# Kernel tuning notes

Hardware: AMD Instinct MI355X
Metric: run time of the kernel (lower is better)

The kernel has to match this reference:

```python
import jax, jax.numpy as jnp
import numpy as np

B = 2048            # number of session graphs in the batch
ORDER = 3           # multi-order granularities s1, s2, s3
D = 128             # input_dim = hidden_dim = output_dim (fc_out is None)
NODES_PER = (50, 25, 16)   # nodes per graph for s1, s2, s3
NPG = sum(NODES_PER)       # 91 nodes per graph (summed batch_num_nodes)
N = B * NPG                # total flattened nodes


def setup_inputs() -> dict:
    key = jax.random.key(0)
    k0, k1, k2, k3 = jax.random.split(key, 4)
    feats = jax.random.normal(k0, (N, D), dtype=jnp.float32)
    scale = 1.0 / np.sqrt(D).astype(np.float32)
    Wu = jax.random.normal(k1, (ORDER, D, D), dtype=jnp.float32) * scale
    bu = jnp.zeros((ORDER, D), dtype=jnp.float32)
    Wv = jax.random.normal(k2, (ORDER, D, D), dtype=jnp.float32) * scale
    We = jax.random.normal(k3, (ORDER, D), dtype=jnp.float32) * scale
    # segment id per node: idx = cat([ones(batch_num_nodes[j]) * j])
    idx = jnp.repeat(jnp.arange(B, dtype=jnp.int32), NPG)
    # last node of each order's block inside every graph (feats['s_i'][last_nodess[i]])
    offs = np.cumsum([0] + list(NODES_PER))
    last = np.stack([np.arange(B) * NPG + (offs[o + 1] - 1) for o in range(ORDER)])
    last_idx = jnp.asarray(last, dtype=jnp.int32)  # [ORDER, B]
    return {"feats": feats, "Wu": Wu, "bu": bu, "Wv": Wv, "We": We,
            "idx": idx, "last_idx": last_idx}


def reference(feats, Wu, bu, Wv, We, idx, last_idx):
    # feat_u = fc_u[i](feats)                        -> [O, N, D]
    feat_u = jnp.einsum('nd,odh->onh', feats, Wu) + bu[:, None, :]
    # feat_v = fc_v[i](feat_vs[:, i])[idx]           -> [O, N, D]
    fv = jnp.einsum('obd,odh->obh', feats[last_idx], Wv)   # [O, B, D]
    feat_v = fv[:, idx, :]                                  # gather per segment id
    # e = fc_e[i](sigmoid(feat_u + feat_v))          -> [N, O]
    e = jnp.einsum('onh,oh->no', jax.nn.sigmoid(feat_u + feat_v), We)
    # alpha = segment_softmax(batch_num_nodes, e), numerically stable
    m = jax.lax.stop_gradient(jax.ops.segment_max(e, idx, num_segments=B))
    ex = jnp.exp(e - m[idx])
    denom = jax.ops.segment_sum(ex, idx, num_segments=B)
    alpha = ex / denom[idx]                                 # [N, O]
    # rst = segment_reduce(batch_num_nodes, feats * alpha, 'sum') -> [B, O, D]
    weighted = alpha[:, :, None] * feats[:, None, :]        # [N, O, D]
    rst = jax.ops.segment_sum(weighted, idx, num_segments=B)
    return rst  # [B, ORDER, D]; fc_out is None and activation is None
```

## Files before the change

### kernel.cpp

```cpp
#include <hip/hip_runtime.h>
#include <hip/hip_bf16.h>
#include <stdint.h>

#define NB 2048
#define D 128
#define NPG 91

typedef __attribute__((ext_vector_type(8))) short short8;
typedef __attribute__((ext_vector_type(4))) float f32x4;

__device__ __forceinline__ unsigned bf16pk(float a, float b) {
  __hip_bfloat162 h2 = __float22bfloat162_rn(make_float2(a, b));
  return *reinterpret_cast<unsigned*>(&h2);
}

__device__ __forceinline__ float sigf(float x) {
  float e = __expf(-x);
  return __builtin_amdgcn_rcpf(1.0f + e);
}

__global__ void w_pack(const float* __restrict__ Wu,
                       const float* __restrict__ Wv,
                       uint4* __restrict__ wpk) {
  const int u = blockIdx.x;
  const float* W = (u < 12) ? Wu : Wv;
  const int uu = (u < 12) ? u : u - 12;
  const int o = uu >> 2, kk = uu & 3;
  const int t = threadIdx.x;
  #pragma unroll
  for (int i = 0; i < 2; ++i) {
    int idx = i * 256 + t;
    int row = idx >> 2, g = idx & 3;
    const float* src = W + (size_t)o * D * D + (kk * 32 + g * 8) * D + row;
    uint4 pk;
    pk.x = bf16pk(src[0 * D], src[1 * D]);
    pk.y = bf16pk(src[2 * D], src[3 * D]);
    pk.z = bf16pk(src[4 * D], src[5 * D]);
    pk.w = bf16pk(src[6 * D], src[7 * D]);
    wpk[(size_t)u * 512 + idx] = pk;
  }
}

__global__ __launch_bounds__(512, 8) void sihg_main(
    const float* __restrict__ feats,
    const uint4* __restrict__ wpk,
    const float* __restrict__ bu,
    const float* __restrict__ We,
    float* __restrict__ out) {
  __shared__ __align__(16) char lds[38528];
  constexpr int FE_OFF  = 0;
  constexpr int BFV_OFF = 24576;
  constexpr int BUL_OFF = 25088;
  constexpr int WEL_OFF = 26624;
  constexpr int EP_OFF  = 28160;
  constexpr int AL_OFF  = 37376;

  const int t = threadIdx.x;
  const int b = blockIdx.x;
  const int q = t >> 6;
  const int l = t & 63;
  const int g = l >> 4;
  const int lm = l & 15;

  float* bfvp = (float*)(lds + BFV_OFF);
  float* bul = (float*)(lds + BUL_OFF);
  float* wel = (float*)(lds + WEL_OFF);
  float (*ep)[3][96] = (float (*)[3][96])(lds + EP_OFF);
  float (*alpha)[96] = (float (*)[96])(lds + AL_OFF);

  const float* fbase = feats + (size_t)b * NPG * D;

  #pragma unroll 1
  for (int i = 0; i < 3; ++i) {
    int c = t + i * 512;
    int r = c >> 4, d0 = (c & 15) * 8;
    uint4 pk4;
    if (r < NPG) {
      const float* src = fbase + r * D + d0;
      float4 f0 = *(const float4*)(src);
      float4 f1 = *(const float4*)(src + 4);
      pk4.x = bf16pk(f0.x, f0.y);
      pk4.y = bf16pk(f0.z, f0.w);
      pk4.z = bf16pk(f1.x, f1.y);
      pk4.w = bf16pk(f1.z, f1.w);
    } else {
      pk4.x = 0u; pk4.y = 0u; pk4.z = 0u; pk4.w = 0u;
    }
    int off = r * 256 + ((d0 * 2) ^ ((r & 7) << 4));
    *(uint4*)(lds + FE_OFF + off) = pk4;
  }
  if (t < 384) {
    bul[t] = bu[t];
    wel[t] = We[t];
  }
  __syncthreads();

  const int LROW[3] = {49, 74, 90};

  #pragma unroll 1
  for (int o = 0; o < 3; ++o) {
    {
      const int frow = LROW[o];
      const int fswz = (frow & 7) << 4;
      f32x4 z = {0.f, 0.f, 0.f, 0.f};
      #pragma unroll
      for (int kk = 0; kk < 4; ++kk) {
        short8 av = *(const short8*)&wpk[(size_t)(12 + o * 4 + kk) * 512 + (q * 16 + lm) * 4 + g];
        short8 bv = *(const short8*)(lds + FE_OFF + frow * 256 + ((kk * 64 + g * 16) ^ fswz));
        z = __builtin_amdgcn_mfma_f32_16x16x32_bf16(av, bv, z, 0, 0, 0);
      }
      if (lm == 0) {
        #pragma unroll
        for (int r = 0; r < 4; ++r)
          bfvp[q * 16 + g * 4 + r] = z[r] + bul[o * 128 + q * 16 + g * 4 + r];
      }
    }
    __syncthreads();

    short8 a[4];
    #pragma unroll
    for (int kk = 0; kk < 4; ++kk)
      a[kk] = *(const short8*)&wpk[(size_t)(o * 4 + kk) * 512 + (q * 16 + lm) * 4 + g];

    #pragma unroll 1
    for (int nh = 0; nh < 2; ++nh) {
      f32x4 acc[3];
      #pragma unroll
      for (int j = 0; j < 3; ++j) acc[j] = (f32x4){0.f, 0.f, 0.f, 0.f};

      #pragma unroll
      for (int kk = 0; kk < 4; ++kk) {
        const int cb = kk * 64 + g * 16;
        #pragma unroll
        for (int j = 0; j < 3; ++j) {
          const int nt = nh * 3 + j;
          short8 bfr = *(const short8*)(lds + FE_OFF + (nt * 16 + lm) * 256 + (cb ^ ((lm & 7) << 4)));
          acc[j] = __builtin_amdgcn_mfma_f32_16x16x32_bf16(a[kk], bfr, acc[j], 0, 0, 0);
        }
      }
      const float* bbp = &bfvp[q * 16 + g * 4];
      const float* wwp = &wel[o * 128 + q * 16 + g * 4];
      #pragma unroll
      for (int j = 0; j < 3; ++j) {
        float e = 0.f;
        #pragma unroll
        for (int r = 0; r < 4; ++r)
          e += sigf(acc[j][r] + bbp[r]) * wwp[r];
        e += __shfl_xor(e, 16);
        e += __shfl_xor(e, 32);
        if (l < 16) ep[q][o][(nh * 3 + j) * 16 + l] = e;
      }
    }
    if (o < 2) __syncthreads();
  }
  __syncthreads();

  if (q < 3) {
    const int o = q;
    const int n1 = l, n2 = l + 64;
    float e1 = -1e30f, e2 = -1e30f;
    if (n1 < NPG) {
      e1 = 0.f;
      #pragma unroll
      for (int j = 0; j < 8; ++j) e1 += ep[j][o][n1];
    }
    if (n2 < NPG) {
      e2 = 0.f;
      #pragma unroll
      for (int j = 0; j < 8; ++j) e2 += ep[j][o][n2];
    }
    float mx = fmaxf(e1, e2);
    #pragma unroll
    for (int m = 1; m < 64; m <<= 1) mx = fmaxf(mx, __shfl_xor(mx, m));
    float x1 = (n1 < NPG) ? __expf(e1 - mx) : 0.f;
    float x2 = (n2 < NPG) ? __expf(e2 - mx) : 0.f;
    float s = x1 + x2;
    #pragma unroll
    for (int m = 1; m < 64; m <<= 1) s += __shfl_xor(s, m);
    float inv = __builtin_amdgcn_rcpf(s);
    if (n1 < NPG) alpha[o][n1] = x1 * inv;
    if (n2 < NPG) alpha[o][n2] = x2 * inv;
  }
  __syncthreads();

  {
    const int hw = t >> 5;
    const int d4 = (t & 31) * 4;
    float a0x = 0.f, a0y = 0.f, a0z = 0.f, a0w = 0.f;
    float a1x = 0.f, a1y = 0.f, a1z = 0.f, a1w = 0.f;
    float a2x = 0.f, a2y = 0.f, a2z = 0.f, a2w = 0.f;
    #pragma unroll 1
    for (int n = hw; n < NPG; n += 16) {
      float4 f = *(const float4*)(fbase + n * D + d4);
      float al0 = alpha[0][n], al1 = alpha[1][n], al2 = alpha[2][n];
      a0x += f.x * al0; a0y += f.y * al0; a0z += f.z * al0; a0w += f.w * al0;
      a1x += f.x * al1; a1y += f.y * al1; a1z += f.z * al1; a1w += f.w * al1;
      a2x += f.x * al2; a2y += f.y * al2; a2z += f.z * al2; a2w += f.w * al2;
    }
    a0x += __shfl_xor(a0x, 32); a0y += __shfl_xor(a0y, 32);
    a0z += __shfl_xor(a0z, 32); a0w += __shfl_xor(a0w, 32);
    a1x += __shfl_xor(a1x, 32); a1y += __shfl_xor(a1y, 32);
    a1z += __shfl_xor(a1z, 32); a1w += __shfl_xor(a1w, 32);
    a2x += __shfl_xor(a2x, 32); a2y += __shfl_xor(a2y, 32);
    a2z += __shfl_xor(a2z, 32); a2w += __shfl_xor(a2w, 32);
    float* part = (float*)(lds + FE_OFF);
    if (l < 32) {
      float4 s0 = {a0x, a0y, a0z, a0w};
      float4 s1 = {a1x, a1y, a1z, a1w};
      float4 s2 = {a2x, a2y, a2z, a2w};
      *(float4*)&part[q * 384 + 0 * 128 + d4] = s0;
      *(float4*)&part[q * 384 + 1 * 128 + d4] = s1;
      *(float4*)&part[q * 384 + 2 * 128 + d4] = s2;
    }
  }
  __syncthreads();
  if (t < 384) {
    const float* part = (const float*)(lds + FE_OFF);
    float s = 0.f;
    #pragma unroll
    for (int j = 0; j < 8; ++j) s += part[j * 384 + t];
    out[(size_t)b * 384 + t] = s;
  }
}

extern "C" void kernel_launch(void* const* d_in, const int* in_sizes, int n_in,
                              void* d_out, int out_size, void* d_ws, size_t ws_size,
                              hipStream_t stream) {
  const float* feats = (const float*)d_in[0];
  const float* Wu    = (const float*)d_in[1];
  const float* bu    = (const float*)d_in[2];
  const float* Wv    = (const float*)d_in[3];
  const float* We    = (const float*)d_in[4];
  float* out = (float*)d_out;
  uint4* wpk = (uint4*)d_ws;

  w_pack<<<24, 256, 0, stream>>>(Wu, Wv, wpk);
  sihg_main<<<NB, 512, 0, stream>>>(feats, wpk, bu, We, out);
}
```

Measured before the change: 65.23 us.

## Hoist feat_v projections for all orders before main loop, drop per-order barriers

Computes the fv projection for all three orders up front into a 384-entry LDS buffer, so a single barrier replaces the two per-order barriers in the main loop. The inner loop now processes all six node tiles at once with six accumulators, loading each weight fragment inline rather than keeping four preloaded. Bias is read directly from global memory with vector loads instead of being staged in LDS. This reduces synchronisation and loop overhead, at the cost of more live accumulator registers, which could lower occupancy.

Measured after the change: 174.5 us. 2.67x slower.

```diff
diff --git a/kernel.cpp b/kernel.cpp
--- a/kernel.cpp
+++ b/kernel.cpp
@@ -47,13 +47,12 @@
     const float* __restrict__ bu,
     const float* __restrict__ We,
     float* __restrict__ out) {
-  __shared__ __align__(16) char lds[38528];
+  __shared__ __align__(16) char lds[38016];
   constexpr int FE_OFF  = 0;
   constexpr int BFV_OFF = 24576;
-  constexpr int BUL_OFF = 25088;
-  constexpr int WEL_OFF = 26624;
-  constexpr int EP_OFF  = 28160;
-  constexpr int AL_OFF  = 37376;
+  constexpr int WEL_OFF = 26112;
+  constexpr int EP_OFF  = 27648;
+  constexpr int AL_OFF  = 36864;
 
   const int t = threadIdx.x;
   const int b = blockIdx.x;
@@ -63,7 +62,6 @@
   const int lm = l & 15;
 
   float* bfvp = (float*)(lds + BFV_OFF);
-  float* bul = (float*)(lds + BUL_OFF);
   float* wel = (float*)(lds + WEL_OFF);
   float (*ep)[3][96] = (float (*)[3][96])(lds + EP_OFF);
   float (*alpha)[96] = (float (*)[96])(lds + AL_OFF);
@@ -89,17 +87,13 @@
     int off = r * 256 + ((d0 * 2) ^ ((r & 7) << 4));
     *(uint4*)(lds + FE_OFF + off) = pk4;
   }
-  if (t < 384) {
-    bul[t] = bu[t];
-    wel[t] = We[t];
-  }
-  __syncthreads();
-
-  const int LROW[3] = {49, 74, 90};
-
-  #pragma unroll 1
-  for (int o = 0; o < 3; ++o) {
-    {
+  if (t < 384) wel[t] = We[t];
+  __syncthreads();
+
+  {
+    const int LROW[3] = {49, 74, 90};
+    #pragma unroll
+    for (int o = 0; o < 3; ++o) {
       const int frow = LROW[o];
       const int fswz = (frow & 7) << 4;
       f32x4 z = {0.f, 0.f, 0.f, 0.f};
@@ -110,48 +104,43 @@
         z = __builtin_amdgcn_mfma_f32_16x16x32_bf16(av, bv, z, 0, 0, 0);
       }
       if (lm == 0) {
-        #pragma unroll
-        for (int r = 0; r < 4; ++r)
-          bfvp[q * 16 + g * 4 + r] = z[r] + bul[o * 128 + q * 16 + g * 4 + r];
+        f32x4 bb = *(const f32x4*)&bu[o * 128 + q * 16 + g * 4];
+        f32x4 s = {z[0] + bb[0], z[1] + bb[1], z[2] + bb[2], z[3] + bb[3]};
+        *(f32x4*)&bfvp[o * 128 + q * 16 + g * 4] = s;
       }
     }
-    __syncthreads();
-
-    short8 a[4];
-    #pragma unroll
-    for (int kk = 0; kk < 4; ++kk)
-      a[kk] = *(const short8*)&wpk[(size_t)(o * 4 + kk) * 512 + (q * 16 + lm) * 4 + g];
-
-    #pragma unroll 1
-    for (int nh = 0; nh < 2; ++nh) {
-      f32x4 acc[3];
-      #pragma unroll
-      for (int j = 0; j < 3; ++j) acc[j] = (f32x4){0.f, 0.f, 0.f, 0.f};
-
-      #pragma unroll
-      for (int kk = 0; kk < 4; ++kk) {
-        const int cb = kk * 64 + g * 16;
-        #pragma unroll
-        for (int j = 0; j < 3; ++j) {
-          const int nt = nh * 3 + j;
-          short8 bfr = *(const short8*)(lds + FE_OFF + (nt * 16 + lm) * 256 + (cb ^ ((lm & 7) << 4)));
-          acc[j] = __builtin_amdgcn_mfma_f32_16x16x32_bf16(a[kk], bfr, acc[j], 0, 0, 0);
-        }
+  }
+  __syncthreads();
+
+  const int swz = (lm & 7) << 4;
+  #pragma unroll 1
+  for (int o = 0; o < 3; ++o) {
+    f32x4 acc[6];
+    #pragma unroll
+    for (int j = 0; j < 6; ++j) acc[j] = (f32x4){0.f, 0.f, 0.f, 0.f};
+
+    #pragma unroll
+    for (int kk = 0; kk < 4; ++kk) {
+      short8 a = *(const short8*)&wpk[(size_t)(o * 4 + kk) * 512 + (q * 16 + lm) * 4 + g];
+      const int cb = kk * 64 + g * 16;
+      #pragma unroll
+      for (int j = 0; j < 6; ++j) {
+        short8 bfr = *(const short8*)(lds + FE_OFF + (j * 16 + lm) * 256 + (cb ^ swz));
+        acc[j] = __builtin_amdgcn_mfma_f32_16x16x32_bf16(a, bfr, acc[j], 0, 0, 0);
       }
-      const float* bbp = &bfvp[q * 16 + g * 4];
-      const float* wwp = &wel[o * 128 + q * 16 + g * 4];
-      #pragma unroll
-      for (int j = 0; j < 3; ++j) {
-        float e = 0.f;
-        #pragma unroll
-        for (int r = 0; r < 4; ++r)
-          e += sigf(acc[j][r] + bbp[r]) * wwp[r];
-        e += __shfl_xor(e, 16);
-        e += __shfl_xor(e, 32);
-        if (l < 16) ep[q][o][(nh * 3 + j) * 16 + l] = e;
-      }
-    }
-    if (o < 2) __syncthreads();
+    }
+    f32x4 bb = *(const f32x4*)&bfvp[o * 128 + q * 16 + g * 4];
+    f32x4 ww = *(const f32x4*)&wel[o * 128 + q * 16 + g * 4];
+    #pragma unroll
+    for (int j = 0; j < 6; ++j) {
+      float e = sigf(acc[j][0] + bb[0]) * ww[0]
+              + sigf(acc[j][1] + bb[1]) * ww[1]
+              + sigf(acc[j][2] + bb[2]) * ww[2]
+              + sigf(acc[j][3] + bb[3]) * ww[3];
+      e += __shfl_xor(e, 16);
+      e += __shfl_xor(e, 32);
+      if (l < 16) ep[q][o][j * 16 + l] = e;
+    }
   }
   __syncthreads();
 
```

## Keep fv bias in registers, drop per-order barriers, prefetch feats for pooling

Applied to the files above, without the earlier changes.

Each wave now keeps the last-node Wv projection plus bias in registers instead of writing it to shared memory, which removes two block barriers per order. The Wu fragments are loaded inside the k loop rather than held as a four-register array. The fp32 feature rows for the final weighted sum are prefetched into registers before the softmax barrier, so the global loads overlap with the softmax. In exchange, register pressure rises (six float4 prefetches are live across the softmax), which could reduce occupancy.

Measured after the change: 60.34 us. -7.5%, faster.

```diff
diff --git a/kernel.cpp b/kernel.cpp
--- a/kernel.cpp
+++ b/kernel.cpp
@@ -47,13 +47,12 @@
     const float* __restrict__ bu,
     const float* __restrict__ We,
     float* __restrict__ out) {
-  __shared__ __align__(16) char lds[38528];
+  __shared__ __align__(16) char lds[38016];
   constexpr int FE_OFF  = 0;
-  constexpr int BFV_OFF = 24576;
-  constexpr int BUL_OFF = 25088;
-  constexpr int WEL_OFF = 26624;
-  constexpr int EP_OFF  = 28160;
-  constexpr int AL_OFF  = 37376;
+  constexpr int BUL_OFF = 24576;
+  constexpr int WEL_OFF = 26112;
+  constexpr int EP_OFF  = 27648;
+  constexpr int AL_OFF  = 36864;
 
   const int t = threadIdx.x;
   const int b = blockIdx.x;
@@ -62,7 +61,6 @@
   const int g = l >> 4;
   const int lm = l & 15;
 
-  float* bfvp = (float*)(lds + BFV_OFF);
   float* bul = (float*)(lds + BUL_OFF);
   float* wel = (float*)(lds + WEL_OFF);
   float (*ep)[3][96] = (float (*)[3][96])(lds + EP_OFF);
@@ -95,32 +93,23 @@
   }
   __syncthreads();
 
-  const int LROW[3] = {49, 74, 90};
-
+  const int swz = (lm & 7) << 4;
   #pragma unroll 1
   for (int o = 0; o < 3; ++o) {
-    {
-      const int frow = LROW[o];
-      const int fswz = (frow & 7) << 4;
-      f32x4 z = {0.f, 0.f, 0.f, 0.f};
-      #pragma unroll
-      for (int kk = 0; kk < 4; ++kk) {
-        short8 av = *(const short8*)&wpk[(size_t)(12 + o * 4 + kk) * 512 + (q * 16 + lm) * 4 + g];
-        short8 bv = *(const short8*)(lds + FE_OFF + frow * 256 + ((kk * 64 + g * 16) ^ fswz));
-        z = __builtin_amdgcn_mfma_f32_16x16x32_bf16(av, bv, z, 0, 0, 0);
-      }
-      if (lm == 0) {
-        #pragma unroll
-        for (int r = 0; r < 4; ++r)
-          bfvp[q * 16 + g * 4 + r] = z[r] + bul[o * 128 + q * 16 + g * 4 + r];
-      }
-    }
-    __syncthreads();
-
-    short8 a[4];
-    #pragma unroll
-    for (int kk = 0; kk < 4; ++kk)
-      a[kk] = *(const short8*)&wpk[(size_t)(o * 4 + kk) * 512 + (q * 16 + lm) * 4 + g];
+    const int frow = (o == 0) ? 49 : (o == 1) ? 74 : 90;
+    const int fswz = (frow & 7) << 4;
+    f32x4 z = {0.f, 0.f, 0.f, 0.f};
+    #pragma unroll
+    for (int kk = 0; kk < 4; ++kk) {
+      short8 av = *(const short8*)&wpk[(size_t)(12 + o * 4 + kk) * 512 + (q * 16 + lm) * 4 + g];
+      short8 bv = *(const short8*)(lds + FE_OFF + frow * 256 + ((kk * 64 + g * 16) ^ fswz));
+      z = __builtin_amdgcn_mfma_f32_16x16x32_bf16(av, bv, z, 0, 0, 0);
+    }
+    f32x4 bu4 = *(const f32x4*)&bul[o * 128 + q * 16 + g * 4];
+    float bias[4];
+    bias[0] = z[0] + bu4[0]; bias[1] = z[1] + bu4[1];
+    bias[2] = z[2] + bu4[2]; bias[3] = z[3] + bu4[3];
+    f32x4 ww = *(const f32x4*)&wel[o * 128 + q * 16 + g * 4];
 
     #pragma unroll 1
     for (int nh = 0; nh < 2; ++nh) {
@@ -130,28 +119,35 @@
 
       #pragma unroll
       for (int kk = 0; kk < 4; ++kk) {
+        short8 a = *(const short8*)&wpk[(size_t)(o * 4 + kk) * 512 + (q * 16 + lm) * 4 + g];
         const int cb = kk * 64 + g * 16;
         #pragma unroll
         for (int j = 0; j < 3; ++j) {
           const int nt = nh * 3 + j;
-          short8 bfr = *(const short8*)(lds + FE_OFF + (nt * 16 + lm) * 256 + (cb ^ ((lm & 7) << 4)));
-          acc[j] = __builtin_amdgcn_mfma_f32_16x16x32_bf16(a[kk], bfr, acc[j], 0, 0, 0);
+          short8 bv = *(const short8*)(lds + FE_OFF + (nt * 16 + lm) * 256 + (cb ^ swz));
+          acc[j] = __builtin_amdgcn_mfma_f32_16x16x32_bf16(a, bv, acc[j], 0, 0, 0);
         }
       }
-      const float* bbp = &bfvp[q * 16 + g * 4];
-      const float* wwp = &wel[o * 128 + q * 16 + g * 4];
       #pragma unroll
       for (int j = 0; j < 3; ++j) {
-        float e = 0.f;
-        #pragma unroll
-        for (int r = 0; r < 4; ++r)
-          e += sigf(acc[j][r] + bbp[r]) * wwp[r];
+        float e = sigf(acc[j][0] + bias[0]) * ww[0]
+                + sigf(acc[j][1] + bias[1]) * ww[1]
+                + sigf(acc[j][2] + bias[2]) * ww[2]
+                + sigf(acc[j][3] + bias[3]) * ww[3];
         e += __shfl_xor(e, 16);
         e += __shfl_xor(e, 32);
         if (l < 16) ep[q][o][(nh * 3 + j) * 16 + l] = e;
       }
     }
-    if (o < 2) __syncthreads();
+  }
+
+  const int hw = t >> 5;
+  const int d4 = (t & 31) * 4;
+  float4 pf[6];
+  #pragma unroll
+  for (int i = 0; i < 6; ++i) {
+    int n = hw + 16 * i;
+    if (n < NPG) pf[i] = *(const float4*)(fbase + n * D + d4);
   }
   __syncthreads();
 
@@ -184,18 +180,18 @@
   __syncthreads();
 
   {
-    const int hw = t >> 5;
-    const int d4 = (t & 31) * 4;
     float a0x = 0.f, a0y = 0.f, a0z = 0.f, a0w = 0.f;
     float a1x = 0.f, a1y = 0.f, a1z = 0.f, a1w = 0.f;
     float a2x = 0.f, a2y = 0.f, a2z = 0.f, a2w = 0.f;
-    #pragma unroll 1
-    for (int n = hw; n < NPG; n += 16) {
-      float4 f = *(const float4*)(fbase + n * D + d4);
-      float al0 = alpha[0][n], al1 = alpha[1][n], al2 = alpha[2][n];
-      a0x += f.x * al0; a0y += f.y * al0; a0z += f.z * al0; a0w += f.w * al0;
-      a1x += f.x * al1; a1y += f.y * al1; a1z += f.z * al1; a1w += f.w * al1;
-      a2x += f.x * al2; a2y += f.y * al2; a2z += f.z * al2; a2w += f.w * al2;
+    #pragma unroll
+    for (int i = 0; i < 6; ++i) {
+      int n = hw + 16 * i;
+      if (n < NPG) {
+        float al0 = alpha[0][n], al1 = alpha[1][n], al2 = alpha[2][n];
+        a0x += pf[i].x * al0; a0y += pf[i].y * al0; a0z += pf[i].z * al0; a0w += pf[i].w * al0;
+        a1x += pf[i].x * al1; a1y += pf[i].y * al1; a1z += pf[i].z * al1; a1w += pf[i].w * al1;
+        a2x += pf[i].x * al2; a2y += pf[i].y * al2; a2z += pf[i].z * al2; a2w += pf[i].w * al2;
+      }
     }
     a0x += __shfl_xor(a0x, 32); a0y += __shfl_xor(a0y, 32);
     a0z += __shfl_xor(a0z, 32); a0w += __shfl_xor(a0w, 32);
```
